# Kernel tuning notes

Hardware: AMD Instinct MI355X
Metric: run time of the kernel (lower is better)

Reference implementation:

```python
import jax, jax.numpy as jnp
import numpy as np

B, S, D, N = 4, 4096, 512, 512  # d_state must equal d_model for the original broadcast to be valid


def setup_inputs() -> dict:
    key = jax.random.key(0)
    ks = jax.random.split(key, 8)
    inv = 1.0 / np.sqrt(D)
    return {
        "x": jax.random.normal(ks[0], (B, S, D), dtype=jnp.float32),
        "state0": jnp.zeros((B, N), dtype=jnp.float32),
        "W_gate": (jax.random.normal(ks[1], (D, D)) * inv).astype(jnp.float32),  # x_proj_gate.weight [out,in]
        "b_gate": jnp.zeros((D,), jnp.float32),
        "W_sp": (jax.random.normal(ks[2], (N, D)) * inv).astype(jnp.float32),    # state_proj.weight [d_state, d_model]
        "b_sp": jnp.zeros((N,), jnp.float32),
        "W_out": (jax.random.normal(ks[3], (D, D)) * inv).astype(jnp.float32),   # out_proj.weight
        "b_out": jnp.zeros((D,), jnp.float32),
        "A_log": (jax.random.normal(ks[4], (D, N)) * 0.02).astype(jnp.float32),
        "D_param": jnp.ones((D,), jnp.float32),
    }


def reference(x, state0, W_gate, b_gate, W_sp, b_sp, W_out, b_out, A_log, D_param):
    # x_gate = silu(x_proj_gate(x))  [B,S,D]
    x_gate = jax.nn.silu(x @ W_gate.T + b_gate)
    # s = state_proj(x_gate)  [B,S,N]
    s = x_gate @ W_sp.T + b_sp
    # A = -exp(A_log); per-step decay = exp(mean_N(A))  [D] (== N by construction)
    A = -jnp.exp(A_log)
    decay = jnp.exp(A.mean(axis=-1))

    def step(state, s_t):  # state [B,N], s_t [B,N]
        state = state * decay + s_t
        return state, state

    state_f, states = jax.lax.scan(step, state0, jnp.swapaxes(s, 0, 1))  # states [S,B,N]
    # y_t = state_t @ state_proj.weight + D * u_t
    y = jnp.einsum('sbn,nd->bsd', states, W_sp) + D_param * x_gate
    out = y @ W_out.T + b_out  # out_proj
    return out, state_f
```

## Files before the change

### kernel.cpp

```cpp
#include <hip/hip_runtime.h>
#include <hip/hip_bf16.h>
#include <stdint.h>


typedef __bf16 bf16_t;
typedef bf16_t bf16x8 __attribute__((ext_vector_type(8)));
typedef bf16_t bf16x4 __attribute__((ext_vector_type(4)));
typedef float  f32x4  __attribute__((ext_vector_type(4)));

static __device__ __forceinline__ void async_copy16(bf16_t* lds, const bf16_t* g) {
    __builtin_amdgcn_global_load_lds((const __attribute__((address_space(1))) void*)g,
                                     (__attribute__((address_space(3))) void*)lds, 16, 0, 0);
}

template <int MODE, int NT, bool SCAN, bool F32A>
__global__ __launch_bounds__(512, 4) void gemm_2ph(
    const void* __restrict__ A0v, const bf16_t* __restrict__ W0,
    const bf16_t* __restrict__ A1, const bf16_t* __restrict__ W1,
    const float* __restrict__ bias, void* __restrict__ outp,
    const float* __restrict__ decay_g, float* __restrict__ carry_g)
{
    constexpr int K = 512;
    __shared__ bf16_t As[2][128 * 64];
    __shared__ bf16_t Bs[2][128 * 64];
    const int tid = threadIdx.x;
    int bid = blockIdx.x;
    {
        int nwg = gridDim.x;
        if ((nwg & 7) == 0) bid = (bid & 7) * (nwg >> 3) + (bid >> 3);
    }
    const int m0 = (bid >> 2) << 7, n0 = (bid & 3) << 7;
    const int l = tid & 63, w = tid >> 6;
    const int wr = w >> 2, wc = w & 3;
    const int lr = l & 15, kc = l >> 4;
    const int rloc = l >> 3, sc = (l & 7) ^ rloc;

    float bv[2];
    #pragma unroll
    for (int j = 0; j < 2; ++j)
        bv[j] = bias ? bias[n0 + wc * 32 + j * 16 + lr] : 0.f;

    f32x4 acc[4][2];
    const f32x4 z = {0.f, 0.f, 0.f, 0.f};
    #pragma unroll
    for (int i = 0; i < 4; ++i)
        #pragma unroll
        for (int j = 0; j < 2; ++j) acc[i][j] = z;

    const bf16_t* __restrict__ A0b = (const bf16_t*)A0v;
    const float*  __restrict__ A0f = (const float*)A0v;
    const int arow = tid >> 2, aq = tid & 3;

    auto stage = [&](int t) {
        const bf16_t* __restrict__ Asrc = (t < 8) ? A0b : A1;
        const bf16_t* __restrict__ Wsrc = (t < 8) ? W0 : W1;
        const int kk = (t & 7) << 6;
        bf16_t* bufA = As[t & 1];
        bf16_t* bufB = Bs[t & 1];
        #pragma unroll
        for (int v = 0; v < 2; ++v) {
            const int win = w * 2 + v;
            async_copy16(bufA + win * 512,
                         Asrc + (size_t)(m0 + win * 8 + rloc) * K + kk + sc * 8);
            async_copy16(bufB + win * 512,
                         Wsrc + (size_t)(n0 + win * 8 + rloc) * K + kk + sc * 8);
        }
    };
    auto stageB = [&](int t) {
        const int kk = (t & 7) << 6;
        bf16_t* bufB = Bs[t & 1];
        #pragma unroll
        for (int v = 0; v < 2; ++v) {
            const int win = w * 2 + v;
            async_copy16(bufB + win * 512,
                         W0 + (size_t)(n0 + win * 8 + rloc) * K + kk + sc * 8);
        }
    };
    float4 arA[4];
    auto issueA = [&](int t) {
        const float* p = A0f + (size_t)(m0 + arow) * K + ((t & 7) << 6) + aq * 16;
        arA[0] = ((const float4*)p)[0];
        arA[1] = ((const float4*)p)[1];
        arA[2] = ((const float4*)p)[2];
        arA[3] = ((const float4*)p)[3];
    };
    auto writeA = [&](int t) {
        bf16x8 v0, v1;
        v0[0]=(bf16_t)arA[0].x; v0[1]=(bf16_t)arA[0].y; v0[2]=(bf16_t)arA[0].z; v0[3]=(bf16_t)arA[0].w;
        v0[4]=(bf16_t)arA[1].x; v0[5]=(bf16_t)arA[1].y; v0[6]=(bf16_t)arA[1].z; v0[7]=(bf16_t)arA[1].w;
        v1[0]=(bf16_t)arA[2].x; v1[1]=(bf16_t)arA[2].y; v1[2]=(bf16_t)arA[2].z; v1[3]=(bf16_t)arA[2].w;
        v1[4]=(bf16_t)arA[3].x; v1[5]=(bf16_t)arA[3].y; v1[6]=(bf16_t)arA[3].z; v1[7]=(bf16_t)arA[3].w;
        bf16_t* bufA = As[t & 1];
        *(bf16x8*)(bufA + arow * 64 + (((aq * 2    ) ^ (arow & 7)) << 3)) = v0;
        *(bf16x8*)(bufA + arow * 64 + (((aq * 2 + 1) ^ (arow & 7)) << 3)) = v1;
    };

    if (F32A) { issueA(0); asm volatile("" ::: "memory"); stageB(0); }
    else      { stage(0); }

    #pragma unroll
    for (int t = 0; t < NT; ++t) {
        if (F32A) {
            asm volatile("s_waitcnt vmcnt(2)" ::: "memory");
            writeA(t);
            if (t + 1 < NT) {
                issueA(t + 1);
                asm volatile("" ::: "memory");
                stageB(t + 1);
                asm volatile("s_waitcnt vmcnt(6) lgkmcnt(0)" ::: "memory");
            } else {
                asm volatile("s_waitcnt vmcnt(0) lgkmcnt(0)" ::: "memory");
            }
        } else {
            if (t + 1 < NT) {
                stage(t + 1);
                asm volatile("s_waitcnt vmcnt(4)" ::: "memory");
            } else {
                asm volatile("s_waitcnt vmcnt(0)" ::: "memory");
            }
        }
        __builtin_amdgcn_s_barrier();
        const bf16_t* __restrict__ bufA = As[t & 1];
        const bf16_t* __restrict__ bufB = Bs[t & 1];
        bf16x8 a[2][4], b[2][2];
        #pragma unroll
        for (int ks = 0; ks < 2; ++ks) {
            #pragma unroll
            for (int i = 0; i < 4; ++i)
                a[ks][i] = *(const bf16x8*)(bufA + (wr * 64 + i * 16 + lr) * 64
                                            + (((ks * 4 + kc) ^ (lr & 7)) << 3));
            #pragma unroll
            for (int j = 0; j < 2; ++j)
                b[ks][j] = *(const bf16x8*)(bufB + (wc * 32 + j * 16 + lr) * 64
                                            + (((ks * 4 + kc) ^ (lr & 7)) << 3));
        }
        #pragma unroll
        for (int ks = 0; ks < 2; ++ks)
            #pragma unroll
            for (int i = 0; i < 4; ++i)
                #pragma unroll
                for (int j = 0; j < 2; ++j)
                    acc[i][j] = __builtin_amdgcn_mfma_f32_16x16x32_bf16(
                        a[ks][i], b[ks][j], acc[i][j], 0, 0, 0);
        if (t + 1 < NT)
            __builtin_amdgcn_s_barrier();
    }

    if (MODE == 0) {
        float* outF = (float*)outp;
        #pragma unroll
        for (int i = 0; i < 4; ++i) {
            const int row = m0 + wr * 64 + i * 16 + kc * 4;
            #pragma unroll
            for (int j = 0; j < 2; ++j) {
                const int col = n0 + wc * 32 + j * 16 + lr;
                #pragma unroll
                for (int r = 0; r < 4; ++r)
                    outF[(size_t)(row + r) * 512 + col] = acc[i][j][r] + bv[j];
            }
        }
    } else {
        __syncthreads();
        bf16_t* eps = &As[0][0];
        #pragma unroll
        for (int i = 0; i < 4; ++i) {
            const int row = wr * 64 + i * 16 + kc * 4;
            #pragma unroll
            for (int j = 0; j < 2; ++j) {
                const int col = wc * 32 + j * 16 + lr;
                #pragma unroll
                for (int r = 0; r < 4; ++r) {
                    float v = acc[i][j][r] + bv[j];
                    if (MODE == 2) v = v / (1.f + __expf(-v));
                    eps[(row + r) * 128 + col] = (bf16_t)v;
                }
            }
        }
        __syncthreads();
        bf16_t* outB = (bf16_t*)outp;
        #pragma unroll
        for (int s2 = 0; s2 < 4; ++s2) {
            const int row = s2 * 32 + (tid >> 4);
            const int col = (tid & 15) * 8;
            *(bf16x8*)(outB + (size_t)(m0 + row) * 512 + n0 + col) =
                *(const bf16x8*)(eps + row * 128 + col);
        }
        if (SCAN) {
            if (tid < 256) {
                const int chalf = tid >> 7, col = tid & 127;
                const int n = n0 + col;
                const float dec = decay_g[n];
                float st = 0.f;
                #pragma unroll 8
                for (int i = 0; i < 64; ++i)
                    st = st * dec + (float)eps[(chalf * 64 + i) * 128 + col];
                carry_g[(size_t)((m0 >> 6) + chalf) * 512 + n] = st;
            }
        }
    }
}

__global__ void prep_all(const float* __restrict__ Wg, const float* __restrict__ Wsp,
                         const float* __restrict__ Wo, const float* __restrict__ Dp,
                         bf16_t* __restrict__ Wg_bf, bf16_t* __restrict__ Wsp_bf,
                         bf16_t* __restrict__ Wo_bf, bf16_t* __restrict__ W2_bf,
                         const float* __restrict__ A_log, float* __restrict__ decay)
{
    const int blk = blockIdx.x, tid = threadIdx.x;
    {
        int i = blk * 256 + tid;
        Wg_bf[i]  = (bf16_t)Wg[i];
        Wsp_bf[i] = (bf16_t)Wsp[i];
        float wo  = Wo[i];
        Wo_bf[i]  = (bf16_t)wo;
        W2_bf[i]  = (bf16_t)(wo * Dp[i & 511]);
    }
    if (blk < 128) {
        int d = blk * 4 + (tid >> 6);
        int ll = tid & 63;
        const float* row = A_log + (size_t)d * 512;
        float s = 0.f;
        for (int k = ll; k < 512; k += 64) s += expf(row[k]);
        #pragma unroll
        for (int off = 32; off > 0; off >>= 1) s += __shfl_down(s, off);
        if (ll == 0) decay[d] = expf(-s * (1.f / 512.f));
    }
}

__global__ void scan_carry(const float* __restrict__ carry, const float* __restrict__ decay,
                           const float* __restrict__ state0,
                           float* __restrict__ exc, float* __restrict__ state_f)
{
    int g = blockIdx.x * 256 + threadIdx.x;
    int n = g & 511, b = g >> 9;
    float dec = decay[n];
    float d64 = dec;
    #pragma unroll
    for (int t = 0; t < 6; ++t) d64 *= d64;
    float st = state0[g];
    for (int ch = 0; ch < 64; ++ch) {
        size_t idx = (size_t)(b * 64 + ch) * 512 + n;
        exc[idx] = st;
        st = st * d64 + carry[idx];
    }
    state_f[g] = st;
}

__global__ void scan_final(const bf16_t* __restrict__ s, const float* __restrict__ decay,
                           const float* __restrict__ exc, bf16_t* __restrict__ states)
{
    int g = blockIdx.x * 256 + threadIdx.x;
    int n = g & 511, ch = (g >> 9) & 63, b = g >> 15;
    float dec = decay[n];
    float st = exc[(size_t)(b * 64 + ch) * 512 + n];
    size_t base = (size_t)(b * 4096 + ch * 64) * 512 + n;
    #pragma unroll 8
    for (int i = 0; i < 64; ++i) {
        st = st * dec + (float)s[base + (size_t)i * 512];
        states[base + (size_t)i * 512] = (bf16_t)st;
    }
}

extern "C" void kernel_launch(void* const* d_in, const int* in_sizes, int n_in,
                              void* d_out, int out_size, void* d_ws, size_t ws_size,
                              hipStream_t stream)
{
    const float* x      = (const float*)d_in[0];
    const float* state0 = (const float*)d_in[1];
    const float* W_gate = (const float*)d_in[2];
    const float* b_gate = (const float*)d_in[3];
    const float* W_sp   = (const float*)d_in[4];
    const float* b_sp   = (const float*)d_in[5];
    const float* W_out  = (const float*)d_in[6];
    const float* b_out  = (const float*)d_in[7];
    const float* A_log  = (const float*)d_in[8];
    const float* D_par  = (const float*)d_in[9];
    float* out = (float*)d_out;

    char* ws = (char*)d_ws;
    bf16_t* states = (bf16_t*)ws;
    bf16_t* xg_bf  = (bf16_t*)(ws + (16u << 20));
    bf16_t* s_bf   = (bf16_t*)(ws + (32u << 20));
    bf16_t* Wg_bf  = (bf16_t*)(ws + (48u << 20));
    bf16_t* Wsp_bf = Wg_bf + 262144;
    bf16_t* Wo_bf  = Wg_bf + 2 * 262144;
    bf16_t* W2_bf  = Wg_bf + 3 * 262144;
    bf16_t* WcT_bf = Wg_bf + 4 * 262144;
    float*  carry  = (float*)(Wg_bf + 5 * 262144);
    float*  exc    = carry + 131072;
    float*  decay  = exc + 131072;

    prep_all<<<dim3(1024), dim3(256), 0, stream>>>(
        W_gate, W_sp, W_out, D_par, Wg_bf, Wsp_bf, Wo_bf, W2_bf, A_log, decay);

    gemm_2ph<1, 8, false, false><<<dim3(16), dim3(512), 0, stream>>>(
        (const void*)Wo_bf, Wsp_bf, (const bf16_t*)nullptr, (const bf16_t*)nullptr,
        (const float*)nullptr, (void*)WcT_bf, (const float*)nullptr, (float*)nullptr);
    gemm_2ph<2, 8, false, true><<<dim3(512), dim3(512), 0, stream>>>(
        (const void*)x, Wg_bf, (const bf16_t*)nullptr, (const bf16_t*)nullptr,
        b_gate, (void*)xg_bf, (const float*)nullptr, (float*)nullptr);
    gemm_2ph<1, 8, true, false><<<dim3(512), dim3(512), 0, stream>>>(
        (const void*)xg_bf, Wsp_bf, (const bf16_t*)nullptr, (const bf16_t*)nullptr,
        b_sp, (void*)s_bf, decay, carry);

    scan_carry<<<dim3(8), dim3(256), 0, stream>>>(carry, decay, state0, exc, out + 8388608);
    scan_final<<<dim3(512), dim3(256), 0, stream>>>(s_bf, decay, exc, states);

    gemm_2ph<0, 16, false, false><<<dim3(512), dim3(512), 0, stream>>>(
        (const void*)states, WcT_bf, xg_bf, W2_bf, b_out, (void*)out,
        (const float*)nullptr, (float*)nullptr);
}
```

Before: 83.15 us.

## Merge WcT GEMM into gate GEMM launch and shorten scan chunks

Turns the GEMM kernel into a device-inlined body so the small W_out·W_sp product runs as 16 extra blocks inside the gate-projection launch, removing one kernel launch. The scan chunk length drops from 64 to 32: the fused GEMM epilogue now uses all 512 threads to compute four carries per tile, scan_carry walks 128 chunks and writes exclusive prefixes in place over the carry buffer, and scan_final processes 8 channels per thread with vectorized bf16x8 loads and stores. The aim is to cut serial scan latency and launch overhead, at the cost of a longer sequential carry pass and fewer threads in the final scan.

```diff
diff --git a/kernel.cpp b/kernel.cpp
--- a/kernel.cpp
+++ b/kernel.cpp
@@ -14,21 +14,16 @@
 }
 
 template <int MODE, int NT, bool SCAN, bool F32A>
-__global__ __launch_bounds__(512, 4) void gemm_2ph(
+static __device__ __forceinline__ void gemm_body(
+    int bid, int nwg, bf16_t* __restrict__ AsB, bf16_t* __restrict__ BsB,
     const void* __restrict__ A0v, const bf16_t* __restrict__ W0,
     const bf16_t* __restrict__ A1, const bf16_t* __restrict__ W1,
     const float* __restrict__ bias, void* __restrict__ outp,
     const float* __restrict__ decay_g, float* __restrict__ carry_g)
 {
     constexpr int K = 512;
-    __shared__ bf16_t As[2][128 * 64];
-    __shared__ bf16_t Bs[2][128 * 64];
     const int tid = threadIdx.x;
-    int bid = blockIdx.x;
-    {
-        int nwg = gridDim.x;
-        if ((nwg & 7) == 0) bid = (bid & 7) * (nwg >> 3) + (bid >> 3);
-    }
+    if ((nwg & 7) == 0) bid = (bid & 7) * (nwg >> 3) + (bid >> 3);
     const int m0 = (bid >> 2) << 7, n0 = (bid & 3) << 7;
     const int l = tid & 63, w = tid >> 6;
     const int wr = w >> 2, wc = w & 3;
@@ -55,8 +50,8 @@
         const bf16_t* __restrict__ Asrc = (t < 8) ? A0b : A1;
         const bf16_t* __restrict__ Wsrc = (t < 8) ? W0 : W1;
         const int kk = (t & 7) << 6;
-        bf16_t* bufA = As[t & 1];
-        bf16_t* bufB = Bs[t & 1];
+        bf16_t* bufA = AsB + (t & 1) * 8192;
+        bf16_t* bufB = BsB + (t & 1) * 8192;
         #pragma unroll
         for (int v = 0; v < 2; ++v) {
             const int win = w * 2 + v;
@@ -68,7 +63,7 @@
     };
     auto stageB = [&](int t) {
         const int kk = (t & 7) << 6;
-        bf16_t* bufB = Bs[t & 1];
+        bf16_t* bufB = BsB + (t & 1) * 8192;
         #pragma unroll
         for (int v = 0; v < 2; ++v) {
             const int win = w * 2 + v;
@@ -90,7 +85,7 @@
         v0[4]=(bf16_t)arA[1].x; v0[5]=(bf16_t)arA[1].y; v0[6]=(bf16_t)arA[1].z; v0[7]=(bf16_t)arA[1].w;
         v1[0]=(bf16_t)arA[2].x; v1[1]=(bf16_t)arA[2].y; v1[2]=(bf16_t)arA[2].z; v1[3]=(bf16_t)arA[2].w;
         v1[4]=(bf16_t)arA[3].x; v1[5]=(bf16_t)arA[3].y; v1[6]=(bf16_t)arA[3].z; v1[7]=(bf16_t)arA[3].w;
-        bf16_t* bufA = As[t & 1];
+        bf16_t* bufA = AsB + (t & 1) * 8192;
         *(bf16x8*)(bufA + arow * 64 + (((aq * 2    ) ^ (arow & 7)) << 3)) = v0;
         *(bf16x8*)(bufA + arow * 64 + (((aq * 2 + 1) ^ (arow & 7)) << 3)) = v1;
     };
@@ -120,8 +115,8 @@
             }
         }
         __builtin_amdgcn_s_barrier();
-        const bf16_t* __restrict__ bufA = As[t & 1];
-        const bf16_t* __restrict__ bufB = Bs[t & 1];
+        const bf16_t* __restrict__ bufA = AsB + (t & 1) * 8192;
+        const bf16_t* __restrict__ bufB = BsB + (t & 1) * 8192;
         bf16x8 a[2][4], b[2][2];
         #pragma unroll
         for (int ks = 0; ks < 2; ++ks) {
@@ -161,7 +156,7 @@
         }
     } else {
         __syncthreads();
-        bf16_t* eps = &As[0][0];
+        bf16_t* eps = AsB;
         #pragma unroll
         for (int i = 0; i < 4; ++i) {
             const int row = wr * 64 + i * 16 + kc * 4;
@@ -186,18 +181,47 @@
                 *(const bf16x8*)(eps + row * 128 + col);
         }
         if (SCAN) {
-            if (tid < 256) {
-                const int chalf = tid >> 7, col = tid & 127;
-                const int n = n0 + col;
-                const float dec = decay_g[n];
-                float st = 0.f;
-                #pragma unroll 8
-                for (int i = 0; i < 64; ++i)
-                    st = st * dec + (float)eps[(chalf * 64 + i) * 128 + col];
-                carry_g[(size_t)((m0 >> 6) + chalf) * 512 + n] = st;
-            }
-        }
-    }
+            const int sub = tid >> 7, col = tid & 127;
+            const int n = n0 + col;
+            const float dec = decay_g[n];
+            float st = 0.f;
+            #pragma unroll 8
+            for (int i = 0; i < 32; ++i)
+                st = st * dec + (float)eps[(sub * 32 + i) * 128 + col];
+            carry_g[(size_t)((m0 >> 5) + sub) * 512 + n] = st;
+        }
+    }
+}
+
+template <int MODE, int NT, bool SCAN, bool F32A>
+__global__ __launch_bounds__(512, 4) void gemm_std(
+    const void* __restrict__ A0v, const bf16_t* __restrict__ W0,
+    const bf16_t* __restrict__ A1, const bf16_t* __restrict__ W1,
+    const float* __restrict__ bias, void* __restrict__ outp,
+    const float* __restrict__ decay_g, float* __restrict__ carry_g)
+{
+    __shared__ bf16_t As[2 * 128 * 64];
+    __shared__ bf16_t Bs[2 * 128 * 64];
+    gemm_body<MODE, NT, SCAN, F32A>(blockIdx.x, gridDim.x, As, Bs,
+                                    A0v, W0, A1, W1, bias, outp, decay_g, carry_g);
+}
+
+__global__ __launch_bounds__(512, 4) void g1_wct(
+    const float* __restrict__ x, const bf16_t* __restrict__ Wg,
+    const float* __restrict__ b_gate, bf16_t* __restrict__ xg,
+    const bf16_t* __restrict__ Wo, const bf16_t* __restrict__ Wsp,
+    bf16_t* __restrict__ WcT)
+{
+    __shared__ bf16_t As[2 * 128 * 64];
+    __shared__ bf16_t Bs[2 * 128 * 64];
+    if (blockIdx.x < 512)
+        gemm_body<2, 8, false, true>(blockIdx.x, 512, As, Bs,
+            (const void*)x, Wg, (const bf16_t*)nullptr, (const bf16_t*)nullptr,
+            b_gate, (void*)xg, (const float*)nullptr, (float*)nullptr);
+    else
+        gemm_body<1, 8, false, false>(blockIdx.x - 512, 16, As, Bs,
+            (const void*)Wo, Wsp, (const bf16_t*)nullptr, (const bf16_t*)nullptr,
+            (const float*)nullptr, (void*)WcT, (const float*)nullptr, (float*)nullptr);
 }
 
 __global__ void prep_all(const float* __restrict__ Wg, const float* __restrict__ Wsp,
@@ -227,37 +251,49 @@
     }
 }
 
-__global__ void scan_carry(const float* __restrict__ carry, const float* __restrict__ decay,
-                           const float* __restrict__ state0,
-                           float* __restrict__ exc, float* __restrict__ state_f)
+__global__ void scan_carry(float* __restrict__ carry, const float* __restrict__ decay,
+                           const float* __restrict__ state0, float* __restrict__ state_f)
 {
     int g = blockIdx.x * 256 + threadIdx.x;
     int n = g & 511, b = g >> 9;
     float dec = decay[n];
-    float d64 = dec;
+    float d32 = dec;
     #pragma unroll
-    for (int t = 0; t < 6; ++t) d64 *= d64;
+    for (int t = 0; t < 5; ++t) d32 *= d32;
     float st = state0[g];
-    for (int ch = 0; ch < 64; ++ch) {
-        size_t idx = (size_t)(b * 64 + ch) * 512 + n;
-        exc[idx] = st;
-        st = st * d64 + carry[idx];
+    for (int ch = 0; ch < 128; ++ch) {
+        size_t idx = (size_t)(b * 128 + ch) * 512 + n;
+        float c = carry[idx];
+        carry[idx] = st;
+        st = st * d32 + c;
     }
     state_f[g] = st;
 }
 
-__global__ void scan_final(const bf16_t* __restrict__ s, const float* __restrict__ decay,
-                           const float* __restrict__ exc, bf16_t* __restrict__ states)
-{
-    int g = blockIdx.x * 256 + threadIdx.x;
-    int n = g & 511, ch = (g >> 9) & 63, b = g >> 15;
-    float dec = decay[n];
-    float st = exc[(size_t)(b * 64 + ch) * 512 + n];
-    size_t base = (size_t)(b * 4096 + ch * 64) * 512 + n;
+__global__ void scan_final8(const bf16_t* __restrict__ s, const float* __restrict__ decay,
+                            const float* __restrict__ exc, bf16_t* __restrict__ states)
+{
+    int g = blockIdx.x * 128 + threadIdx.x;
+    int ng = g & 63, ch = (g >> 6) & 127, b = g >> 13;
+    const int n0 = ng * 8;
+    float4 d0 = *(const float4*)(decay + n0);
+    float4 d1 = *(const float4*)(decay + n0 + 4);
+    const float* ep = exc + (size_t)(b * 128 + ch) * 512 + n0;
+    float4 s0 = *(const float4*)ep;
+    float4 s1 = *(const float4*)(ep + 4);
+    float st[8] = {s0.x, s0.y, s0.z, s0.w, s1.x, s1.y, s1.z, s1.w};
+    const float dc[8] = {d0.x, d0.y, d0.z, d0.w, d1.x, d1.y, d1.z, d1.w};
+    size_t base = (size_t)(b * 4096 + ch * 32) * 512 + n0;
     #pragma unroll 8
-    for (int i = 0; i < 64; ++i) {
-        st = st * dec + (float)s[base + (size_t)i * 512];
-        states[base + (size_t)i * 512] = (bf16_t)st;
+    for (int i = 0; i < 32; ++i) {
+        bf16x8 v = *(const bf16x8*)(s + base + (size_t)i * 512);
+        bf16x8 o;
+        #pragma unroll
+        for (int k = 0; k < 8; ++k) {
+            st[k] = st[k] * dc[k] + (float)v[k];
+            o[k] = (bf16_t)st[k];
+        }
+        *(bf16x8*)(states + base + (size_t)i * 512) = o;
     }
 }
 
@@ -287,26 +323,22 @@
     bf16_t* W2_bf  = Wg_bf + 3 * 262144;
     bf16_t* WcT_bf = Wg_bf + 4 * 262144;
     float*  carry  = (float*)(Wg_bf + 5 * 262144);
-    float*  exc    = carry + 131072;
-    float*  decay  = exc + 131072;
+    float*  decay  = carry + 262144;
 
     prep_all<<<dim3(1024), dim3(256), 0, stream>>>(
         W_gate, W_sp, W_out, D_par, Wg_bf, Wsp_bf, Wo_bf, W2_bf, A_log, decay);
 
-    gemm_2ph<1, 8, false, false><<<dim3(16), dim3(512), 0, stream>>>(
-        (const void*)Wo_bf, Wsp_bf, (const bf16_t*)nullptr, (const bf16_t*)nullptr,
-        (const float*)nullptr, (void*)WcT_bf, (const float*)nullptr, (float*)nullptr);
-    gemm_2ph<2, 8, false, true><<<dim3(512), dim3(512), 0, stream>>>(
-        (const void*)x, Wg_bf, (const bf16_t*)nullptr, (const bf16_t*)nullptr,
-        b_gate, (void*)xg_bf, (const float*)nullptr, (float*)nullptr);
-    gemm_2ph<1, 8, true, false><<<dim3(512), dim3(512), 0, stream>>>(
+    g1_wct<<<dim3(528), dim3(512), 0, stream>>>(
+        x, Wg_bf, b_gate, xg_bf, Wo_bf, Wsp_bf, WcT_bf);
+
+    gemm_std<1, 8, true, false><<<dim3(512), dim3(512), 0, stream>>>(
         (const void*)xg_bf, Wsp_bf, (const bf16_t*)nullptr, (const bf16_t*)nullptr,
         b_sp, (void*)s_bf, decay, carry);
 
-    scan_carry<<<dim3(8), dim3(256), 0, stream>>>(carry, decay, state0, exc, out + 8388608);
-    scan_final<<<dim3(512), dim3(256), 0, stream>>>(s_bf, decay, exc, states);
-
-    gemm_2ph<0, 16, false, false><<<dim3(512), dim3(512), 0, stream>>>(
+    scan_carry<<<dim3(8), dim3(256), 0, stream>>>(carry, decay, state0, out + 8388608);
+    scan_final8<<<dim3(256), dim3(128), 0, stream>>>(s_bf, decay, carry, states);
+
+    gemm_std<0, 16, false, false><<<dim3(512), dim3(512), 0, stream>>>(
         (const void*)states, WcT_bf, xg_bf, W2_bf, b_out, (void*)out,
         (const float*)nullptr, (float*)nullptr);
 }
```

New measurement: 83.44 us. No clear change (+0.4%).
